# Kernel optimization log

Hardware: AMD Instinct MI355X
Metric: run time of the kernel (lower is better)

## Reference

```python
import jax, jax.numpy as jnp
import numpy as np

K = 5          # kernel_size per pseudo-dim
KK = K * K     # 25 weight slots (dim=2)
NUM_GRAPHS = 64


def spline_conv(x, src, dst, pseudo, W, root, bias):
    """SplineConv, degree-1 open B-spline, dim=2, aggr='mean', root weight + bias.
    x: [N, I], pseudo: [E, 2] in [0,1], W: [KK, I, O], root: [I, O], bias: [O].
    """
    N = x.shape[0]
    E = src.shape[0]
    O = W.shape[-1]
    # degree-1 open spline: v = u * (K-1); linear interpolation between knots
    v = pseudo * (K - 1)                      # [E, 2]
    bot = jnp.floor(v)
    frac = v - bot                            # [E, 2]
    bot = bot.astype(jnp.int32)
    # precompute per-node transform for every kernel slot: [N, KK, O] -> flat [N*KK, O]
    Xk = jnp.einsum('ni,kio->nko', x, W).reshape(N * KK, O)
    msg = jnp.zeros((E, O), x.dtype)
    for s0 in (0, 1):
        b0 = frac[:, 0] if s0 else 1.0 - frac[:, 0]
        i0 = jnp.clip(bot[:, 0] + s0, 0, K - 1)
        for s1 in (0, 1):
            b1 = frac[:, 1] if s1 else 1.0 - frac[:, 1]
            i1 = jnp.clip(bot[:, 1] + s1, 0, K - 1)
            flat = src * KK + i0 * K + i1     # [E] gather index into Xk
            msg = msg + (b0 * b1)[:, None] * Xk[flat]
    # mean aggregation over incoming edges
    agg = jax.ops.segment_sum(msg, dst, num_segments=N)
    deg = jax.ops.segment_sum(jnp.ones((E,), x.dtype), dst, num_segments=N)
    agg = agg / jnp.maximum(deg, 1.0)[:, None]
    return agg + x @ root + bias


def batch_average(x, batch, num_graphs):
    s = jax.ops.segment_sum(x, batch, num_segments=num_graphs)
    c = jax.ops.segment_sum(jnp.ones((x.shape[0],), x.dtype), batch, num_segments=num_graphs)
    return s / jnp.maximum(c, 1.0)[:, None]


def setup_inputs() -> dict:
    key = jax.random.key(0)
    ks = jax.random.split(key, 16)
    N, E = 30000, 600000
    x = jax.random.normal(ks[0], (N, 8), dtype=jnp.float32)
    edge_index = jax.random.randint(ks[1], (2, E), 0, N, dtype=jnp.int64)
    pseudo = jax.random.uniform(ks[2], (E, 2), dtype=jnp.float32)
    batch = jnp.sort(jax.random.randint(ks[3], (N,), 0, NUM_GRAPHS, dtype=jnp.int64))

    def glorot(k, shape):
        fan = shape[-2] + shape[-1]
        return jax.random.normal(k, shape, dtype=jnp.float32) * np.sqrt(2.0 / fan)

    return {
        'x': x, 'edge_index': edge_index, 'pseudo': pseudo, 'batch': batch,
        'W1': glorot(ks[4], (KK, 8, 32)),   'root1': glorot(ks[5], (8, 32)),   'b1': jnp.zeros((32,), jnp.float32),
        'W2': glorot(ks[6], (KK, 32, 64)),  'root2': glorot(ks[7], (32, 64)),  'b2': jnp.zeros((64,), jnp.float32),
        'W3': glorot(ks[8], (KK, 64, 124)), 'root3': glorot(ks[9], (64, 124)), 'b3': jnp.zeros((124,), jnp.float32),
        'fc_w': glorot(ks[10], (124, 30)),  'fc_b': jnp.zeros((30,), jnp.float32),
    }


def reference(x, edge_index, pseudo, batch,
              W1, root1, b1, W2, root2, b2, W3, root3, b3, fc_w, fc_b):
    src = edge_index[0].astype(jnp.int32)
    dst = edge_index[1].astype(jnp.int32)
    batch32 = batch.astype(jnp.int32)
    h = jax.nn.elu(spline_conv(x, src, dst, pseudo, W1, root1, b1))
    h = jax.nn.elu(spline_conv(h, src, dst, pseudo, W2, root2, b2))
    h = jax.nn.elu(spline_conv(h, src, dst, pseudo, W3, root3, b3))
    g = batch_average(h, batch32, NUM_GRAPHS)        # [G, 124]
    # dropout is identity in eval mode
    logits = g @ fc_w + fc_b                         # [G, 30]
    return jax.nn.log_softmax(logits, axis=-1)
```

## Files before the change

kernel.cpp:

```cpp
#include <hip/hip_runtime.h>
#include <cstdint>
#include <cstddef>

#define KKSLOTS 25

typedef __attribute__((ext_vector_type(8))) short short8;
typedef __attribute__((ext_vector_type(4))) float f32x4;
typedef __attribute__((ext_vector_type(4))) unsigned short us4;

__device__ __forceinline__ unsigned short f2bf(float f) {
    unsigned u = __float_as_uint(f);
    u += 0x7FFF + ((u >> 16) & 1);
    return (unsigned short)(u >> 16);
}
__device__ __forceinline__ float bf2f(unsigned short b) {
    return __uint_as_float((unsigned)b << 16);
}

__global__ void csr_count_kernel(const int* __restrict__ dst, int* __restrict__ cnt, int E) {
    int e = blockIdx.x * blockDim.x + threadIdx.x;
    if (e < E) atomicAdd(&cnt[dst[e]], 1);
}

#define SCAN_B 256
__global__ __launch_bounds__(SCAN_B) void scan1_kernel(const int* __restrict__ cnt,
                                                       int* __restrict__ off,
                                                       int* __restrict__ bsum, int N) {
    __shared__ int tmp[SCAN_B];
    int g = blockIdx.x * SCAN_B + threadIdx.x;
    int v = (g < N) ? cnt[g] : 0;
    tmp[threadIdx.x] = v;
    __syncthreads();
    for (int d = 1; d < SCAN_B; d <<= 1) {
        int t = (threadIdx.x >= d) ? tmp[threadIdx.x - d] : 0;
        __syncthreads();
        tmp[threadIdx.x] += t;
        __syncthreads();
    }
    if (g < N) off[g] = tmp[threadIdx.x] - v;
    if (threadIdx.x == SCAN_B - 1) bsum[blockIdx.x] = tmp[threadIdx.x];
}

__global__ __launch_bounds__(SCAN_B) void scan2_kernel(int* __restrict__ bsum, int nb) {
    __shared__ int tmp[SCAN_B];
    int v = (threadIdx.x < nb) ? bsum[threadIdx.x] : 0;
    tmp[threadIdx.x] = v;
    __syncthreads();
    for (int d = 1; d < SCAN_B; d <<= 1) {
        int t = (threadIdx.x >= d) ? tmp[threadIdx.x - d] : 0;
        __syncthreads();
        tmp[threadIdx.x] += t;
        __syncthreads();
    }
    if (threadIdx.x < nb) bsum[threadIdx.x] = tmp[threadIdx.x] - v;
}

__global__ void scan3_kernel(int* __restrict__ off, const int* __restrict__ bsum, int N) {
    int g = blockIdx.x * SCAN_B + threadIdx.x;
    if (g < N) off[g] += bsum[blockIdx.x];
}

__global__ void csr_fill_kernel(const int* __restrict__ src, const int* __restrict__ dst,
                                const float* __restrict__ pseudo,
                                int* __restrict__ off, int4* __restrict__ rec, int E) {
    int e = blockIdx.x * blockDim.x + threadIdx.x;
    if (e >= E) return;
    int d = dst[e];
    int p = atomicAdd(&off[d], 1);
    float v0 = pseudo[2 * e + 0] * 4.0f;
    float v1 = pseudo[2 * e + 1] * 4.0f;
    float fl0 = floorf(v0), fl1 = floorf(v1);
    float f0 = v0 - fl0, f1 = v1 - fl1;
    int b0 = (int)fl0, b1 = (int)fl1;
    int i0a = min(max(b0, 0), 4),     i1a = min(max(b1, 0), 4);
    int i0b = min(max(b0 + 1, 0), 4), i1b = min(max(b1 + 1, 0), 4);
    int s00 = i0a * 5 + i1a;
    int s01 = i0a * 5 + i1b;
    int s10 = i0b * 5 + i1a;
    int s11 = i0b * 5 + i1b;
    int packed = s00 | (s01 << 5) | (s10 << 10) | (s11 << 15);
    int4 r;
    r.x = src[e];
    r.y = packed;
    r.z = __float_as_int(f0);
    r.w = __float_as_int(f1);
    rec[p] = r;
}

__global__ void to_bf16_kernel(const float* __restrict__ in, unsigned short* __restrict__ out, int n) {
    int i = blockIdx.x * 256 + threadIdx.x;
    if (i < n) out[i] = f2bf(in[i]);
}

template<int KP, int I, int O, int OP>
__global__ void build_wt_kernel(const float* __restrict__ W, const float* __restrict__ root,
                                unsigned short* __restrict__ WT) {
    int idx = blockIdx.x * 256 + threadIdx.x;
    if (idx >= OP * KP) return;
    int o = idx / KP, k = idx - o * KP;
    float v = 0.0f;
    if (o < O) {
        if (k < KKSLOTS * I) v = W[(size_t)k * O + o];
        else if (k < (KKSLOTS + 1) * I) v = root[(size_t)(k - KKSLOTS * I) * O + o];
    }
    WT[idx] = f2bf(v);
}

template<int I>
__device__ __forceinline__ void edge_add(float* la, int lane, int4 r,
                                         const unsigned short* __restrict__ xb) {
    float f0 = __int_as_float(r.z), f1 = __int_as_float(r.w);
    float g0 = 1.0f - f0, g1 = 1.0f - f1;
    int pk = r.y;
    if constexpr (I == 64) {
        float xv = bf2f(xb[(size_t)r.x * 64 + lane]);
        la[((pk      ) & 31) * 64 + lane] += g0 * g1 * xv;
        la[((pk >> 5 ) & 31) * 64 + lane] += g0 * f1 * xv;
        la[((pk >> 10) & 31) * 64 + lane] += f0 * g1 * xv;
        la[((pk >> 15) & 31) * 64 + lane] += f0 * f1 * xv;
    } else if constexpr (I == 32) {
        int ch = lane & 31, half = lane >> 5;
        float xv = bf2f(xb[(size_t)r.x * 32 + ch]);
        float wA = half ? f0 : g0;
        int sh = half * 10;
        int sA = (pk >> sh) & 31, sB = (pk >> (sh + 5)) & 31;
        la[sA * 32 + ch] += wA * g1 * xv;
        la[sB * 32 + ch] += wA * f1 * xv;
    } else {
        int ch = lane & 7, corner = (lane >> 3) & 3;
        if (lane < 32) {
            float xv = bf2f(xb[(size_t)r.x * 8 + ch]);
            int s = (pk >> (corner * 5)) & 31;
            float w = ((corner & 2) ? f0 : g0) * ((corner & 1) ? f1 : g1);
            la[s * 8 + ch] += w * xv;
        }
    }
}

template<int I, int KP>
__global__ __launch_bounds__(256) void seg_accum_kernel(
        const unsigned short* __restrict__ xb, const int4* __restrict__ rec,
        const int* __restrict__ off, unsigned short* __restrict__ accB,
        int nlo, int nhi) {
    constexpr int SLOTS = KKSLOTS * I;
    __shared__ float la_all[4][SLOTS];
    int wline = threadIdx.x >> 6, lane = threadIdx.x & 63;
    float* la = la_all[wline];
    int wid = blockIdx.x * 4 + wline;
    int nwt = gridDim.x << 2;

    int e_lo = (nlo == 0) ? 0 : off[nlo - 1];
    int e_hi = off[nhi - 1];
    long long span = (long long)e_hi - e_lo;
    int t0 = e_lo + (int)(span * wid / nwt);
    int t1 = e_lo + (int)(span * (wid + 1) / nwt);

    int ns, ne;
    {   int lo = nlo, hi = nhi;
        while (lo < hi) { int m = (lo + hi) >> 1; if (off[m] > t0) hi = m; else lo = m + 1; }
        ns = (wid == 0) ? nlo : lo; }
    {   int lo = nlo, hi = nhi;
        while (lo < hi) { int m = (lo + hi) >> 1; if (off[m] > t1) hi = m; else lo = m + 1; }
        ne = (wid == nwt - 1) ? nhi : lo; }
    if (ns >= ne) return;

    for (int t = lane; t < SLOTS; t += 64) la[t] = 0.0f;
    int j = (ns == 0) ? 0 : off[ns - 1];
    for (int n = ns; n < ne; ++n) {
        int je = off[n];
        int jstart = j;
        while (j + 4 <= je) {
            int4 r0 = rec[j], r1 = rec[j + 1], r2 = rec[j + 2], r3 = rec[j + 3];
            edge_add<I>(la, lane, r0, xb);
            edge_add<I>(la, lane, r1, xb);
            edge_add<I>(la, lane, r2, xb);
            edge_add<I>(la, lane, r3, xb);
            j += 4;
        }
        while (j < je) { edge_add<I>(la, lane, rec[j], xb); ++j; }

        float dinv = 1.0f / fmaxf((float)(je - jstart), 1.0f);
        unsigned short* drow = accB + (size_t)(n - nlo) * KP;
        for (int t = lane; t < SLOTS; t += 64) drow[t] = f2bf(la[t] * dinv);
        for (int t = SLOTS + lane; t < KP; t += 64) {
            int ii = t - SLOTS;
            drow[t] = (ii < I) ? xb[(size_t)n * I + ii] : (unsigned short)0;
        }
        for (int t = lane; t < SLOTS; t += 64) la[t] = 0.0f;
    }
}

template<int KP, int O, int OP>
__global__ __launch_bounds__(256) void contract_mfma_kernel(
        const unsigned short* __restrict__ accB, const unsigned short* __restrict__ WT,
        const float* __restrict__ bias, unsigned short* __restrict__ hout,
        int nlo, int nhi) {
    constexpr int NF = OP / 16;
    constexpr int LDW = 40;
    __shared__ unsigned short wTl[OP][LDW];
    int tid = threadIdx.x;
    int wv = tid >> 6, lane = tid & 63;
    int quad = lane >> 4, l16 = lane & 15;
    int n0 = nlo + blockIdx.x * 64;

    int an = n0 + wv * 16 + l16;
    int arow = min(an, nhi - 1) - nlo;

    f32x4 acc[NF];
    #pragma unroll
    for (int t = 0; t < NF; ++t) acc[t] = (f32x4){0.0f, 0.0f, 0.0f, 0.0f};

    for (int k0 = 0; k0 < KP; k0 += 32) {
        for (int t = tid; t < OP * 8; t += 256) {
            int o = t >> 3;
            int kk = (t & 7) * 4;
            *(us4*)&wTl[o][kk] = *(const us4*)&WT[(size_t)o * KP + k0 + kk];
        }
        __syncthreads();
        short8 a = *(const short8*)(accB + (size_t)arow * KP + k0 + quad * 8);
        #pragma unroll
        for (int t = 0; t < NF; ++t) {
            short8 b = *(const short8*)&wTl[t * 16 + l16][quad * 8];
            acc[t] = __builtin_amdgcn_mfma_f32_16x16x32_bf16(a, b, acc[t], 0, 0, 0);
        }
        __syncthreads();
    }

    #pragma unroll
    for (int t = 0; t < NF; ++t) {
        int o = t * 16 + l16;
        if (o >= O) continue;
        float bs = bias[o];
        #pragma unroll
        for (int r = 0; r < 4; ++r) {
            int n = n0 + wv * 16 + quad * 4 + r;
            if (n >= nhi) continue;
            float v = acc[t][r] + bs;
            v = (v > 0.0f) ? v : expm1f(v);
            hout[(size_t)n * O + o] = f2bf(v);
        }
    }
}

#define GS_CH 128
__global__ __launch_bounds__(128) void graph_reduce_kernel(
        const unsigned short* __restrict__ h3, const int* __restrict__ batch,
        float* __restrict__ g, int N) {
    int o = threadIdx.x;
    if (o >= 124) return;
    int n0 = blockIdx.x * GS_CH;
    int n1 = min(n0 + GS_CH, N);
    float local = 0.0f;
    int cur_b = batch[n0];
    for (int n = n0; n < n1; ++n) {
        int b = batch[n];
        if (b != cur_b) {
            atomicAdd(&g[cur_b * 124 + o], local);
            local = 0.0f;
            cur_b = b;
        }
        local += bf2f(h3[(size_t)n * 124 + o]);
    }
    atomicAdd(&g[cur_b * 124 + o], local);
}

__global__ __launch_bounds__(256) void batch_count_kernel(
        const int* __restrict__ batch, float* __restrict__ cnt, int N) {
    __shared__ int hist[64];
    int tid = threadIdx.x;
    if (tid < 64) hist[tid] = 0;
    __syncthreads();
    int n = blockIdx.x * blockDim.x + tid;
    if (n < N) atomicAdd(&hist[batch[n]], 1);
    __syncthreads();
    if (tid < 64 && hist[tid] > 0) atomicAdd(&cnt[tid], (float)hist[tid]);
}

__global__ void head_kernel(const float* __restrict__ g, const float* __restrict__ cnt,
                            const float* __restrict__ fcw, const float* __restrict__ fcb,
                            float* __restrict__ out) {
    __shared__ float logits[32];
    __shared__ float red[2];
    int b = blockIdx.x;
    int o = threadIdx.x;
    float c = fmaxf(cnt[b], 1.0f);
    if (o < 30) {
        float a = fcb[o];
        for (int i = 0; i < 124; ++i)
            a = fmaf(g[b * 124 + i] / c, fcw[i * 30 + o], a);
        logits[o] = a;
    }
    __syncthreads();
    if (o == 0) {
        float m = -1e30f;
        for (int j = 0; j < 30; ++j) m = fmaxf(m, logits[j]);
        float s = 0.0f;
        for (int j = 0; j < 30; ++j) s += expf(logits[j] - m);
        red[0] = m;
        red[1] = logf(s);
    }
    __syncthreads();
    if (o < 30) out[b * 30 + o] = logits[o] - red[0] - red[1];
}

template<int I, int O, int OP>
static void run_layer(const unsigned short* hb, const unsigned short* WT, const float* bias,
                      unsigned short* hout, unsigned short* accB,
                      const int4* rec, const int* off,
                      int N, size_t avail, hipStream_t stream) {
    constexpr int KP = ((26 * I + 31) / 32) * 32;
    size_t perNode = (size_t)KP * 2;
    size_t maxNodesS = avail / perNode;
    int maxNodes = (maxNodesS > (size_t)N) ? N : (int)maxNodesS;
    if (maxNodes < 64) maxNodes = 64;
    for (int nlo = 0; nlo < N; nlo += maxNodes) {
        int nhi = nlo + maxNodes;
        if (nhi > N) nhi = N;
        int cn = nhi - nlo;
        seg_accum_kernel<I, KP><<<1024, 256, 0, stream>>>(hb, rec, off, accB, nlo, nhi);
        contract_mfma_kernel<KP, O, OP><<<(cn + 63) / 64, 256, 0, stream>>>(
            accB, WT, bias, hout, nlo, nhi);
    }
}

extern "C" void kernel_launch(void* const* d_in, const int* in_sizes, int n_in,
                              void* d_out, int out_size, void* d_ws, size_t ws_size,
                              hipStream_t stream) {
    const float* x      = (const float*)d_in[0];
    const int*   ei     = (const int*)  d_in[1];
    const float* pseudo = (const float*)d_in[2];
    const int*   batch  = (const int*)  d_in[3];
    const float* W1 = (const float*)d_in[4];
    const float* r1 = (const float*)d_in[5];
    const float* b1 = (const float*)d_in[6];
    const float* W2 = (const float*)d_in[7];
    const float* r2 = (const float*)d_in[8];
    const float* b2 = (const float*)d_in[9];
    const float* W3 = (const float*)d_in[10];
    const float* r3 = (const float*)d_in[11];
    const float* b3 = (const float*)d_in[12];
    const float* fcw = (const float*)d_in[13];
    const float* fcb = (const float*)d_in[14];

    int N = in_sizes[0] / 8;
    int E = in_sizes[1] / 2;
    const int* srcp = ei;
    const int* dstp = ei + E;

    constexpr int KP1 = 224, KP2 = 832, KP3 = 1664;

    char* p = (char*)d_ws;
    unsigned short* xb  = (unsigned short*)p; p += (size_t)N * 8 * 2;
    unsigned short* h1  = (unsigned short*)p; p += (size_t)N * 32 * 2;
    unsigned short* h2  = (unsigned short*)p; p += (size_t)N * 64 * 2;
    unsigned short* h3  = (unsigned short*)p; p += (size_t)N * 124 * 2;
    float* gbuf = (float*)p; p += 64 * 124 * 4;
    float* cntF = (float*)p; p += 256;
    int*   cntI = (int*)p;   p += ((size_t)N * 4 + 15) & ~15ULL;
    int*   off  = (int*)p;   p += ((size_t)N * 4 + 15) & ~15ULL;
    int*   bsum = (int*)p;   p += SCAN_B * 4;
    int4*  rec  = (int4*)p;  p += (size_t)E * 16;
    unsigned short* WT1 = (unsigned short*)p; p += (size_t)32  * KP1 * 2;
    unsigned short* WT2 = (unsigned short*)p; p += (size_t)64  * KP2 * 2;
    unsigned short* WT3 = (unsigned short*)p; p += (size_t)128 * KP3 * 2;
    unsigned short* accB = (unsigned short*)p;
    size_t used = (size_t)(p - (char*)d_ws);
    size_t avail = (ws_size > used) ? (ws_size - used) : 0;

    hipMemsetAsync(gbuf, 0, 64 * 124 * 4 + 256 + (((size_t)N * 4 + 15) & ~15ULL), stream);

    int nb_scan = (N + SCAN_B - 1) / SCAN_B;
    csr_count_kernel<<<(E + 255) / 256, 256, 0, stream>>>(dstp, cntI, E);
    scan1_kernel<<<nb_scan, SCAN_B, 0, stream>>>(cntI, off, bsum, N);
    scan2_kernel<<<1, SCAN_B, 0, stream>>>(bsum, nb_scan);
    scan3_kernel<<<nb_scan, SCAN_B, 0, stream>>>(off, bsum, N);
    csr_fill_kernel<<<(E + 255) / 256, 256, 0, stream>>>(srcp, dstp, pseudo, off, rec, E);

    to_bf16_kernel<<<(N * 8 + 255) / 256, 256, 0, stream>>>(x, xb, N * 8);
    build_wt_kernel<KP1, 8,  32,  32 ><<<(32  * KP1 + 255) / 256, 256, 0, stream>>>(W1, r1, WT1);
    build_wt_kernel<KP2, 32, 64,  64 ><<<(64  * KP2 + 255) / 256, 256, 0, stream>>>(W2, r2, WT2);
    build_wt_kernel<KP3, 64, 124, 128><<<(128 * KP3 + 255) / 256, 256, 0, stream>>>(W3, r3, WT3);

    run_layer<8,  32,  32 >(xb, WT1, b1, h1, accB, rec, off, N, avail, stream);
    run_layer<32, 64,  64 >(h1, WT2, b2, h2, accB, rec, off, N, avail, stream);
    run_layer<64, 124, 128>(h2, WT3, b3, h3, accB, rec, off, N, avail, stream);

    graph_reduce_kernel<<<(N + GS_CH - 1) / GS_CH, 128, 0, stream>>>(h3, batch, gbuf, N);
    batch_count_kernel<<<(N + 255) / 256, 256, 0, stream>>>(batch, cntF, N);
    head_kernel<<<64, 64, 0, stream>>>(gbuf, cntF, fcw, fcb, (float*)d_out);
}
```

Measured before the change: 506.8 us.

## Restructure edge accumulation lanes with vectorized corners and dual LDS tiles

Edge scattering is remapped so each lane owns one spline corner and four channels, using 4-wide vector loads of source features and 4-wide vector LDS updates. For I=8 and I=32 two edges are processed at once into separate LDS tiles that are summed at writeback. The writeback now emits packed bf16 pairs. The grid doubles to 2048 blocks, and graph node counting is folded into the graph reduce kernel so one launch is removed. The cost is double the LDS tile for the small layers and some wasted lanes on odd-degree tails.

New measurement: 558.1 us. 10.1% more time.

```diff
diff --git a/kernel.cpp b/kernel.cpp
--- a/kernel.cpp
+++ b/kernel.cpp
@@ -107,33 +107,24 @@
 }
 
 template<int I>
-__device__ __forceinline__ void edge_add(float* la, int lane, int4 r,
-                                         const unsigned short* __restrict__ xb) {
+__device__ __forceinline__ void edge_proc(float* lat, int chb, int sh, bool selA, bool selB,
+                                          int4 r, const unsigned short* __restrict__ xb,
+                                          float scale) {
     float f0 = __int_as_float(r.z), f1 = __int_as_float(r.w);
-    float g0 = 1.0f - f0, g1 = 1.0f - f1;
-    int pk = r.y;
-    if constexpr (I == 64) {
-        float xv = bf2f(xb[(size_t)r.x * 64 + lane]);
-        la[((pk      ) & 31) * 64 + lane] += g0 * g1 * xv;
-        la[((pk >> 5 ) & 31) * 64 + lane] += g0 * f1 * xv;
-        la[((pk >> 10) & 31) * 64 + lane] += f0 * g1 * xv;
-        la[((pk >> 15) & 31) * 64 + lane] += f0 * f1 * xv;
-    } else if constexpr (I == 32) {
-        int ch = lane & 31, half = lane >> 5;
-        float xv = bf2f(xb[(size_t)r.x * 32 + ch]);
-        float wA = half ? f0 : g0;
-        int sh = half * 10;
-        int sA = (pk >> sh) & 31, sB = (pk >> (sh + 5)) & 31;
-        la[sA * 32 + ch] += wA * g1 * xv;
-        la[sB * 32 + ch] += wA * f1 * xv;
+    float w = (selA ? f0 : 1.0f - f0) * (selB ? f1 : 1.0f - f1) * scale;
+    int slot = (r.y >> sh) & 31;
+    if constexpr (I == 8) {
+        float xv = bf2f(xb[(size_t)r.x * 8 + chb]);
+        lat[slot * 8 + chb] += w * xv;
     } else {
-        int ch = lane & 7, corner = (lane >> 3) & 3;
-        if (lane < 32) {
-            float xv = bf2f(xb[(size_t)r.x * 8 + ch]);
-            int s = (pk >> (corner * 5)) & 31;
-            float w = ((corner & 2) ? f0 : g0) * ((corner & 1) ? f1 : g1);
-            la[s * 8 + ch] += w * xv;
-        }
+        us4 xr = *(const us4*)&xb[(size_t)r.x * I + chb];
+        float* d = lat + slot * I + chb;
+        f32x4 v = *(f32x4*)d;
+        v[0] += w * bf2f(xr[0]);
+        v[1] += w * bf2f(xr[1]);
+        v[2] += w * bf2f(xr[2]);
+        v[3] += w * bf2f(xr[3]);
+        *(f32x4*)d = v;
     }
 }
 
@@ -143,7 +134,9 @@
         const int* __restrict__ off, unsigned short* __restrict__ accB,
         int nlo, int nhi) {
     constexpr int SLOTS = KKSLOTS * I;
-    __shared__ float la_all[4][SLOTS];
+    constexpr bool DUAL = (I != 64);
+    constexpr int TILE = DUAL ? 2 * SLOTS : SLOTS;
+    __shared__ __align__(16) float la_all[4][TILE];
     int wline = threadIdx.x >> 6, lane = threadIdx.x & 63;
     float* la = la_all[wline];
     int wid = blockIdx.x * 4 + wline;
@@ -164,29 +157,57 @@
         ne = (wid == nwt - 1) ? nhi : lo; }
     if (ns >= ne) return;
 
-    for (int t = lane; t < SLOTS; t += 64) la[t] = 0.0f;
+    int corner, chb;
+    float* lat;
+    if constexpr (I == 64)      { corner = lane >> 4;        chb = (lane & 15) * 4; lat = la; }
+    else if constexpr (I == 32) { corner = (lane >> 3) & 3;  chb = (lane & 7) * 4;  lat = la + (lane >> 5) * SLOTS; }
+    else                        { corner = (lane >> 3) & 3;  chb = lane & 7;        lat = la + (lane >> 5) * SLOTS; }
+    int sh = corner * 5;
+    bool selA = (corner & 2) != 0, selB = (corner & 1) != 0;
+    int h = lane >> 5;
+
+    for (int t = lane; t < TILE; t += 64) la[t] = 0.0f;
+
     int j = (ns == 0) ? 0 : off[ns - 1];
     for (int n = ns; n < ne; ++n) {
         int je = off[n];
         int jstart = j;
-        while (j + 4 <= je) {
-            int4 r0 = rec[j], r1 = rec[j + 1], r2 = rec[j + 2], r3 = rec[j + 3];
-            edge_add<I>(la, lane, r0, xb);
-            edge_add<I>(la, lane, r1, xb);
-            edge_add<I>(la, lane, r2, xb);
-            edge_add<I>(la, lane, r3, xb);
-            j += 4;
-        }
-        while (j < je) { edge_add<I>(la, lane, rec[j], xb); ++j; }
+        if constexpr (!DUAL) {
+            while (j + 2 <= je) {
+                int4 r0 = rec[j], r1 = rec[j + 1];
+                edge_proc<I>(lat, chb, sh, selA, selB, r0, xb, 1.0f);
+                edge_proc<I>(lat, chb, sh, selA, selB, r1, xb, 1.0f);
+                j += 2;
+            }
+            if (j < je) { edge_proc<I>(lat, chb, sh, selA, selB, rec[j], xb, 1.0f); ++j; }
+        } else {
+            while (j < je) {
+                int idx = j + h;
+                int cl = min(idx, je - 1);
+                int4 r = rec[cl];
+                float scale = (idx < je) ? 1.0f : 0.0f;
+                edge_proc<I>(lat, chb, sh, selA, selB, r, xb, scale);
+                j += 2;
+            }
+            j = je;
+        }
 
         float dinv = 1.0f / fmaxf((float)(je - jstart), 1.0f);
-        unsigned short* drow = accB + (size_t)(n - nlo) * KP;
-        for (int t = lane; t < SLOTS; t += 64) drow[t] = f2bf(la[t] * dinv);
-        for (int t = SLOTS + lane; t < KP; t += 64) {
-            int ii = t - SLOTS;
-            drow[t] = (ii < I) ? xb[(size_t)n * I + ii] : (unsigned short)0;
-        }
-        for (int t = lane; t < SLOTS; t += 64) la[t] = 0.0f;
+        unsigned* drow = (unsigned*)(accB + (size_t)(n - nlo) * KP);
+        const unsigned* hrow = (const unsigned*)(xb + (size_t)n * I);
+        for (int t = lane; t < KP / 2; t += 64) {
+            int e0 = 2 * t;
+            if (e0 < SLOTS) {
+                float v0 = la[e0], v1 = la[e0 + 1];
+                if constexpr (DUAL) { v0 += la[SLOTS + e0]; v1 += la[SLOTS + e0 + 1]; }
+                v0 *= dinv; v1 *= dinv;
+                drow[t] = (unsigned)f2bf(v0) | ((unsigned)f2bf(v1) << 16);
+            } else {
+                int ii = e0 - SLOTS;
+                drow[t] = (ii < I) ? hrow[ii >> 1] : 0u;
+            }
+        }
+        for (int t = lane; t < TILE; t += 64) la[t] = 0.0f;
     }
 }
 
@@ -245,35 +266,37 @@
 #define GS_CH 128
 __global__ __launch_bounds__(128) void graph_reduce_kernel(
         const unsigned short* __restrict__ h3, const int* __restrict__ batch,
-        float* __restrict__ g, int N) {
+        float* __restrict__ g, float* __restrict__ cnt, int N) {
     int o = threadIdx.x;
-    if (o >= 124) return;
     int n0 = blockIdx.x * GS_CH;
     int n1 = min(n0 + GS_CH, N);
-    float local = 0.0f;
-    int cur_b = batch[n0];
-    for (int n = n0; n < n1; ++n) {
-        int b = batch[n];
-        if (b != cur_b) {
-            atomicAdd(&g[cur_b * 124 + o], local);
-            local = 0.0f;
-            cur_b = b;
-        }
-        local += bf2f(h3[(size_t)n * 124 + o]);
-    }
-    atomicAdd(&g[cur_b * 124 + o], local);
-}
-
-__global__ __launch_bounds__(256) void batch_count_kernel(
-        const int* __restrict__ batch, float* __restrict__ cnt, int N) {
-    __shared__ int hist[64];
-    int tid = threadIdx.x;
-    if (tid < 64) hist[tid] = 0;
-    __syncthreads();
-    int n = blockIdx.x * blockDim.x + tid;
-    if (n < N) atomicAdd(&hist[batch[n]], 1);
-    __syncthreads();
-    if (tid < 64 && hist[tid] > 0) atomicAdd(&cnt[tid], (float)hist[tid]);
+    if (o < 124) {
+        float local = 0.0f;
+        int cur_b = batch[n0];
+        for (int n = n0; n < n1; ++n) {
+            int b = batch[n];
+            if (b != cur_b) {
+                atomicAdd(&g[cur_b * 124 + o], local);
+                local = 0.0f;
+                cur_b = b;
+            }
+            local += bf2f(h3[(size_t)n * 124 + o]);
+        }
+        atomicAdd(&g[cur_b * 124 + o], local);
+    } else if (o == 124) {
+        float localc = 0.0f;
+        int cur_b = batch[n0];
+        for (int n = n0; n < n1; ++n) {
+            int b = batch[n];
+            if (b != cur_b) {
+                atomicAdd(&cnt[cur_b], localc);
+                localc = 0.0f;
+                cur_b = b;
+            }
+            localc += 1.0f;
+        }
+        atomicAdd(&cnt[cur_b], localc);
+    }
 }
 
 __global__ void head_kernel(const float* __restrict__ g, const float* __restrict__ cnt,
@@ -317,7 +340,7 @@
         int nhi = nlo + maxNodes;
         if (nhi > N) nhi = N;
         int cn = nhi - nlo;
-        seg_accum_kernel<I, KP><<<1024, 256, 0, stream>>>(hb, rec, off, accB, nlo, nhi);
+        seg_accum_kernel<I, KP><<<2048, 256, 0, stream>>>(hb, rec, off, accB, nlo, nhi);
         contract_mfma_kernel<KP, O, OP><<<(cn + 63) / 64, 256, 0, stream>>>(
             accB, WT, bias, hout, nlo, nhi);
     }
@@ -385,7 +408,6 @@
     run_layer<32, 64,  64 >(h1, WT2, b2, h2, accB, rec, off, N, avail, stream);
     run_layer<64, 124, 128>(h2, WT3, b3, h3, accB, rec, off, N, avail, stream);
 
-    graph_reduce_kernel<<<(N + GS_CH - 1) / GS_CH, 128, 0, stream>>>(h3, batch, gbuf, N);
-    batch_count_kernel<<<(N + 255) / 256, 256, 0, stream>>>(batch, cntF, N);
+    graph_reduce_kernel<<<(N + GS_CH - 1) / GS_CH, 128, 0, stream>>>(h3, batch, gbuf, cntF, N);
     head_kernel<<<64, 64, 0, stream>>>(gbuf, cntF, fcw, fcb, (float*)d_out);
 }
```
